# Kernel optimization log

Hardware: AMD Instinct MI355X
Metric: run time of the kernel (lower is better)

Reference implementation:

```python
import jax, jax.numpy as jnp
import numpy as np

D, H, L, V, BS = 1024, 16, 12, 50257, 2048
HD = D // H
EPS = 1e-5


def _ln(x, w, b):
    m = jnp.mean(x, -1, keepdims=True)
    v = jnp.mean(jnp.square(x - m), -1, keepdims=True)
    return (x - m) * jax.lax.rsqrt(v + EPS) * w + b


def setup_inputs() -> dict:
    key = jax.random.key(0)
    ks = jax.random.split(key, 10)
    B, T = 4, 1024
    s = 0.02
    return {
        "idx": jax.random.randint(ks[0], (B, T), 0, V),
        "targets": jax.random.randint(ks[1], (B, T), 0, V),
        "wte": s * jax.random.normal(ks[2], (V, D), jnp.float32),
        "wpe": s * jax.random.normal(ks[3], (BS, D), jnp.float32),
        "ln1_w": jnp.ones((L, D), jnp.float32),
        "ln1_b": jnp.zeros((L, D), jnp.float32),
        "qkv_w": s * jax.random.normal(ks[4], (L, D, 3 * D), jnp.float32),
        "qkv_b": jnp.zeros((L, 3 * D), jnp.float32),
        "o_w": s * jax.random.normal(ks[5], (L, D, D), jnp.float32),
        "o_b": jnp.zeros((L, D), jnp.float32),
        "ln2_w": jnp.ones((L, D), jnp.float32),
        "ln2_b": jnp.zeros((L, D), jnp.float32),
        "up_w": s * jax.random.normal(ks[6], (L, D, 4 * D), jnp.float32),
        "up_b": jnp.zeros((L, 4 * D), jnp.float32),
        "down_w": s * jax.random.normal(ks[7], (L, 4 * D, D), jnp.float32),
        "down_b": jnp.zeros((L, D), jnp.float32),
        "lnf_w": jnp.ones((D,), jnp.float32),
        "lnf_b": jnp.zeros((D,), jnp.float32),
        "lm_b": jnp.zeros((V,), jnp.float32),
    }


def _gpt(idx, targets, wte, wpe, ln1_w, ln1_b, qkv_w, qkv_b, o_w, o_b,
         ln2_w, ln2_b, up_w, up_b, down_w, down_b, lnf_w, lnf_b, lm_b):
    B, T = idx.shape
    x = wte[idx] + wpe[:T][None, :, :]  # [B,T,D]
    causal = jnp.tril(jnp.ones((T, T), bool))
    scale = HD ** -0.5

    def block(h, p):
        (l1w, l1b, qw, qb, ow, ob, l2w, l2b, uw, ub, dw, db) = p
        y = _ln(h, l1w, l1b)
        qkv = y @ qw + qb  # [B,T,3D]
        q, k, v = jnp.split(qkv, 3, axis=-1)
        q = q.reshape(B, T, H, HD)
        k = k.reshape(B, T, H, HD)
        v = v.reshape(B, T, H, HD)
        scores = jnp.einsum('bqhd,bkhd->bhqk', q, k) * scale
        scores = jnp.where(causal, scores, -jnp.inf)
        attn = jax.nn.softmax(scores, axis=-1)
        o = jnp.einsum('bhqk,bkhd->bqhd', attn, v).reshape(B, T, D)
        h = h + o @ ow + ob
        y = _ln(h, l2w, l2b)
        y = jax.nn.gelu(y @ uw + ub, approximate=False)
        h = h + y @ dw + db
        return h, None

    params = (ln1_w, ln1_b, qkv_w, qkv_b, o_w, o_b, ln2_w, ln2_b, up_w, up_b, down_w, down_b)
    x, _ = jax.lax.scan(block, x, params)
    x = _ln(x, lnf_w, lnf_b)
    logits = x @ wte.T + lm_b  # tied lm_head weight
    logp = jax.nn.log_softmax(logits, axis=-1)
    nll = -jnp.take_along_axis(logp, targets[..., None], axis=-1)[..., 0]
    loss = jnp.mean(nll)
    return logits, loss


def reference(idx, targets, wte, wpe, ln1_w, ln1_b, qkv_w, qkv_b, o_w, o_b,
              ln2_w, ln2_b, up_w, up_b, down_w, down_b, lnf_w, lnf_b, lm_b):
    return _gpt(idx, targets, wte, wpe, ln1_w, ln1_b, qkv_w, qkv_b, o_w, o_b,
                ln2_w, ln2_b, up_w, up_b, down_w, down_b, lnf_w, lnf_b, lm_b)
```

## Files before the change

kernel.cpp:

```cpp
#include <hip/hip_runtime.h>
#include <hip/hip_bf16.h>
#include <math.h>

typedef __attribute__((ext_vector_type(8))) short bfrag;
typedef __attribute__((ext_vector_type(4))) float f32x4;

static constexpr int Dm = 1024, Hh = 16, HD = 64, Ll = 12, Tt = 1024, Bb = 4;
static constexpr int Vv = 50257, Mrows = 4096;
static constexpr int PLD = 200;

__device__ inline unsigned short f2bf(float f) {
    unsigned u = __float_as_uint(f);
    u += 0x7fffu + ((u >> 16) & 1u);
    return (unsigned short)(u >> 16);
}
__device__ inline float bf2f(unsigned short s) {
    return __uint_as_float(((unsigned)s) << 16);
}

__device__ inline void gload16(const unsigned short* g, unsigned short* l) {
    __builtin_amdgcn_global_load_lds(
        (const __attribute__((address_space(1))) void*)g,
        (__attribute__((address_space(3))) void*)l, 16, 0, 0);
}

__global__ __launch_bounds__(256)
void embed_kernel(float* __restrict__ x, const float* __restrict__ wte,
                  const float* __restrict__ wpe, const int* __restrict__ idx) {
    int row = blockIdx.x;
    int t = row & (Tt - 1);
    int id = idx[row];
    int c = threadIdx.x * 4;
    float4 a = *reinterpret_cast<const float4*>(&wte[(size_t)id * Dm + c]);
    float4 p = *reinterpret_cast<const float4*>(&wpe[(size_t)t * Dm + c]);
    float4 o;
    o.x = a.x + p.x; o.y = a.y + p.y; o.z = a.z + p.z; o.w = a.w + p.w;
    *reinterpret_cast<float4*>(&x[(size_t)row * Dm + c]) = o;
}

__global__ __launch_bounds__(256)
void ln_kernel(unsigned short* __restrict__ y, const float* __restrict__ x,
               const float* __restrict__ w, const float* __restrict__ b) {
    int row = blockIdx.x;
    int tid = threadIdx.x;
    int lane = tid & 63, wv = tid >> 6;
    const float* xr = x + (size_t)row * Dm;
    float4 v = *reinterpret_cast<const float4*>(&xr[tid * 4]);
    float s1 = v.x + v.y + v.z + v.w;
    float s2 = v.x * v.x + v.y * v.y + v.z * v.z + v.w * v.w;
#pragma unroll
    for (int off = 1; off < 64; off <<= 1) {
        s1 += __shfl_xor(s1, off);
        s2 += __shfl_xor(s2, off);
    }
    __shared__ float r1[4], r2[4];
    if (lane == 0) { r1[wv] = s1; r2[wv] = s2; }
    __syncthreads();
    s1 = r1[0] + r1[1] + r1[2] + r1[3];
    s2 = r2[0] + r2[1] + r2[2] + r2[3];
    float mean = s1 * (1.0f / Dm);
    float var = s2 * (1.0f / Dm) - mean * mean;
    float rstd = rsqrtf(var + 1e-5f);
    float4 wvv = *reinterpret_cast<const float4*>(&w[tid * 4]);
    float4 bv = *reinterpret_cast<const float4*>(&b[tid * 4]);
    ushort4 o;
    o.x = f2bf((v.x - mean) * rstd * wvv.x + bv.x);
    o.y = f2bf((v.y - mean) * rstd * wvv.y + bv.y);
    o.z = f2bf((v.z - mean) * rstd * wvv.z + bv.z);
    o.w = f2bf((v.w - mean) * rstd * wvv.w + bv.w);
    *reinterpret_cast<ushort4*>(&y[(size_t)row * Dm + tid * 4]) = o;
}

__global__ __launch_bounds__(256)
void transpose_layer(const float* __restrict__ qw, const float* __restrict__ ow,
                     const float* __restrict__ uw, const float* __restrict__ dw,
                     unsigned short* __restrict__ wTq, unsigned short* __restrict__ wTo,
                     unsigned short* __restrict__ wTu, unsigned short* __restrict__ wTd) {
    __shared__ float t[32][33];
    int tb = blockIdx.x;
    const float* src; unsigned short* dst; int K, N, nx, base;
    if (tb < 3072)      { src = qw; dst = wTq; K = 1024; N = 3072; nx = 96;  base = 0; }
    else if (tb < 4096) { src = ow; dst = wTo; K = 1024; N = 1024; nx = 32;  base = 3072; }
    else if (tb < 8192) { src = uw; dst = wTu; K = 1024; N = 4096; nx = 128; base = 4096; }
    else                { src = dw; dst = wTd; K = 4096; N = 1024; nx = 32;  base = 8192; }
    int tt = tb - base;
    int n0 = (tt % nx) * 32, k0 = (tt / nx) * 32;
    int tid = threadIdx.x;
    int r = tid >> 3, c4 = (tid & 7) * 4;
    float4 v = *reinterpret_cast<const float4*>(&src[(size_t)(k0 + r) * N + n0 + c4]);
    t[r][c4] = v.x; t[r][c4 + 1] = v.y; t[r][c4 + 2] = v.z; t[r][c4 + 3] = v.w;
    __syncthreads();
    int nr = tid >> 3, kc = (tid & 7) * 4;
    ushort4 o;
    o.x = f2bf(t[kc][nr]);
    o.y = f2bf(t[kc + 1][nr]);
    o.z = f2bf(t[kc + 2][nr]);
    o.w = f2bf(t[kc + 3][nr]);
    *reinterpret_cast<ushort4*>(&dst[(size_t)(n0 + nr) * K + k0 + kc]) = o;
}

__global__ __launch_bounds__(128)
void cvt_rows(unsigned short* __restrict__ dst, const float* __restrict__ src) {
    int row = blockIdx.x;
    int t = threadIdx.x;
    const float* s = src + (size_t)row * Dm + t * 8;
    float4 f0 = *reinterpret_cast<const float4*>(s);
    float4 f1 = *reinterpret_cast<const float4*>(s + 4);
    ushort4 o0, o1;
    o0.x = f2bf(f0.x); o0.y = f2bf(f0.y); o0.z = f2bf(f0.z); o0.w = f2bf(f0.w);
    o1.x = f2bf(f1.x); o1.y = f2bf(f1.y); o1.z = f2bf(f1.z); o1.w = f2bf(f1.w);
    unsigned short* d = dst + (size_t)row * Dm + t * 8;
    *reinterpret_cast<ushort4*>(d) = o0;
    *reinterpret_cast<ushort4*>(d + 4) = o1;
}

template<int EPI, int GN>
__global__ __launch_bounds__(512, 1)
void gemm256p8(const unsigned short* __restrict__ A, const unsigned short* __restrict__ B,
               const float* __restrict__ bias, void* __restrict__ Cp,
               int Nv, int K, int ldc, int ncol,
               float* __restrict__ pm_out, float* __restrict__ ps_out) {
    __shared__ unsigned short AL[2][2][8192];
    __shared__ unsigned short BL[2][2][8192];
    const int tid = threadIdx.x;
    const int lane = tid & 63, w = tid >> 6;
    const int wr = w >> 2, wc = w & 3;
    const int g = lane >> 4, lr = lane & 15;

    const int gx = gridDim.x;
    const int ny = GN ? ((Nv + 255) >> 8) : (int)gridDim.y;
    int s = blockIdx.y * gx + blockIdx.x;
    int xcd = s & 7, t0b = s >> 3;
    int xblk = t0b % gx, istr = t0b / gx;
    int y = xcd + (istr << 3);
    if (GN && y >= ny) return;
    const int bm = xblk * 256;
    const int bn = y * 256;

    const int srow = tid >> 3;
    const int gsrc = (tid & 7) ^ (srow & 7);
    size_t aofs[2][2], bofs[2][2];
#pragma unroll
    for (int h = 0; h < 2; ++h)
#pragma unroll
        for (int j = 0; j < 2; ++j) {
            int ra = bm + h * 128 + srow + j * 64;
            aofs[h][j] = (size_t)ra * K + gsrc * 8;
            int rb = bn + h * 128 + srow + j * 64;
            if (GN) rb = (rb < Nv) ? rb : (Nv - 1);
            bofs[h][j] = (size_t)rb * K + gsrc * 8;
        }
    const int dst0 = tid * 8, dst1 = tid * 8 + 4096;

    const int nt = K >> 6;
    const int ni = nt >> 1;

    f32x4 acc[8][4];
#pragma unroll
    for (int i = 0; i < 8; ++i)
#pragma unroll
        for (int j = 0; j < 4; ++j)
#pragma unroll
            for (int r = 0; r < 4; ++r) acc[i][j][r] = 0.f;

#define STG_A(d, h, kt) do { \
        gload16(A + aofs[h][0] + ((size_t)(kt) << 6), &AL[d][h][dst0]); \
        gload16(A + aofs[h][1] + ((size_t)(kt) << 6), &AL[d][h][dst1]); } while (0)
#define STG_B(d, h, kt) do { \
        gload16(B + bofs[h][0] + ((size_t)(kt) << 6), &BL[d][h][dst0]); \
        gload16(B + bofs[h][1] + ((size_t)(kt) << 6), &BL[d][h][dst1]); } while (0)

    STG_B(0, 0, 0); STG_B(0, 1, 0);
    STG_A(0, 0, 0); STG_A(0, 1, 0);
    STG_B(1, 0, 1); STG_B(1, 1, 1);
    asm volatile("s_waitcnt vmcnt(0)" ::: "memory");
    asm volatile("s_barrier" ::: "memory");

    const unsigned short* alw[2] = { &AL[0][wr][0], &AL[1][wr][0] };
    const unsigned short* blw[2] = { &BL[0][wc >> 1][0], &BL[1][wc >> 1][0] };
    const int rbB = (wc & 1) * 64;

    bfrag bfr[4][2], afr[2][2];

    for (int i = 0; i < ni; ++i) {
        const int t1 = 2 * i + 1;
        const int tp0 = 2 * i + 2, tp1 = 2 * i + 3;
        const bool pf = (tp0 < nt);
#pragma unroll
        for (int q = 0; q < 4; ++q) {
            if (q == 0) {
#pragma unroll
                for (int n_ = 0; n_ < 4; ++n_)
#pragma unroll
                    for (int ks = 0; ks < 2; ++ks) {
                        int row = rbB + n_ * 16 + lr;
                        int sg = (ks * 4 + g) ^ (row & 7);
                        bfr[n_][ks] = *reinterpret_cast<const bfrag*>(&blw[0][row * 64 + sg * 8]);
                    }
            }
#pragma unroll
            for (int m2 = 0; m2 < 2; ++m2)
#pragma unroll
                for (int ks = 0; ks < 2; ++ks) {
                    int row = q * 32 + m2 * 16 + lr;
                    int sg = (ks * 4 + g) ^ (row & 7);
                    afr[m2][ks] = *reinterpret_cast<const bfrag*>(&alw[0][row * 64 + sg * 8]);
                }
            if (q == 0)      { STG_A(1, 0, t1); }
            else if (q == 1) { STG_A(1, 1, t1); }
            else if (q == 2) { if (pf) STG_B(0, 0, tp0); }
            else             { if (pf) STG_B(0, 1, tp0); }
            asm volatile("s_barrier" ::: "memory");
            __builtin_amdgcn_s_setprio(1);
#pragma unroll
            for (int m2 = 0; m2 < 2; ++m2)
#pragma unroll
                for (int n_ = 0; n_ < 4; ++n_)
#pragma unroll
                    for (int ks = 0; ks < 2; ++ks)
                        acc[q * 2 + m2][n_] = __builtin_amdgcn_mfma_f32_16x16x32_bf16(
                            afr[m2][ks], bfr[n_][ks], acc[q * 2 + m2][n_], 0, 0, 0);
            __builtin_amdgcn_s_setprio(0);
            if (q == 3) {
                if (i + 1 < ni) asm volatile("s_waitcnt vmcnt(4)" ::: "memory");
                else            asm volatile("s_waitcnt vmcnt(0)" ::: "memory");
            }
            asm volatile("s_barrier" ::: "memory");
        }
#pragma unroll
        for (int q = 0; q < 4; ++q) {
            if (q == 0) {
#pragma unroll
                for (int n_ = 0; n_ < 4; ++n_)
#pragma unroll
                    for (int ks = 0; ks < 2; ++ks) {
                        int row = rbB + n_ * 16 + lr;
                        int sg = (ks * 4 + g) ^ (row & 7);
                        bfr[n_][ks] = *reinterpret_cast<const bfrag*>(&blw[1][row * 64 + sg * 8]);
                    }
            }
#pragma unroll
            for (int m2 = 0; m2 < 2; ++m2)
#pragma unroll
                for (int ks = 0; ks < 2; ++ks) {
                    int row = q * 32 + m2 * 16 + lr;
                    int sg = (ks * 4 + g) ^ (row & 7);
                    afr[m2][ks] = *reinterpret_cast<const bfrag*>(&alw[1][row * 64 + sg * 8]);
                }
            if (q == 0)      { if (pf) STG_A(0, 0, tp0); }
            else if (q == 1) { if (pf) STG_A(0, 1, tp0); }
            else if (q == 2) { if (tp1 < nt) STG_B(1, 0, tp1); }
            else             { if (tp1 < nt) STG_B(1, 1, tp1); }
            asm volatile("s_barrier" ::: "memory");
            __builtin_amdgcn_s_setprio(1);
#pragma unroll
            for (int m2 = 0; m2 < 2; ++m2)
#pragma unroll
                for (int n_ = 0; n_ < 4; ++n_)
#pragma unroll
                    for (int ks = 0; ks < 2; ++ks)
                        acc[q * 2 + m2][n_] = __builtin_amdgcn_mfma_f32_16x16x32_bf16(
                            afr[m2][ks], bfr[n_][ks], acc[q * 2 + m2][n_], 0, 0, 0);
            __builtin_amdgcn_s_setprio(0);
            if (q == 3 && i + 1 < ni) asm volatile("s_waitcnt vmcnt(4)" ::: "memory");
            asm volatile("s_barrier" ::: "memory");
        }
    }
#undef STG_A
#undef STG_B

    unsigned short* Cb = (unsigned short*)Cp;
    float* Cf = (float*)Cp;

    if (EPI == 1) {
#pragma unroll
        for (int n_ = 0; n_ < 4; ++n_) {
            int col = bn + wc * 64 + n_ * 16 + lr;
            int gcol = ncol + col;
            float bi = bias[gcol];
#pragma unroll
            for (int mi = 0; mi < 8; ++mi) {
                int row0 = bm + wr * 128 + mi * 16 + g * 4;
#pragma unroll
                for (int r = 0; r < 4; ++r) {
                    int row = row0 + r;
                    float v = acc[mi][n_][r] + bi;
                    v = 0.5f * v * (1.0f + erff(v * 0.70710678118654752f));
                    Cb[(size_t)row * ldc + gcol] = f2bf(v);
                }
            }
        }
    } else {
        __syncthreads();
        float* lm = (float*)&AL[0][0][0];
        float* lsd = lm + 1024;
        float bi4[4];
        int colv[4];
#pragma unroll
        for (int n_ = 0; n_ < 4; ++n_) {
            colv[n_] = bn + wc * 64 + n_ * 16 + lr;
            bi4[n_] = (colv[n_] < Nv) ? bias[ncol + colv[n_]] : 0.f;
        }
#pragma unroll
        for (int mi = 0; mi < 8; ++mi) {
#pragma unroll
            for (int r = 0; r < 4; ++r) {
                int row = bm + wr * 128 + mi * 16 + g * 4 + r;
                float vv[4];
                float ml = -3.0e38f, sl = 0.f;
#pragma unroll
                for (int n_ = 0; n_ < 4; ++n_) {
                    float v = acc[mi][n_][r] + bi4[n_];
                    vv[n_] = v;
                    if (colv[n_] < Nv) ml = fmaxf(ml, v);
                }
#pragma unroll
                for (int n_ = 0; n_ < 4; ++n_) {
                    if (colv[n_] < Nv) {
                        sl += __expf(vv[n_] - ml);
                        __builtin_nontemporal_store(
                            vv[n_], &Cf[(size_t)row * ldc + ncol + colv[n_]]);
                    }
                }
#pragma unroll
                for (int off = 1; off < 16; off <<= 1) {
                    float om = __shfl_xor(ml, off);
                    float os = __shfl_xor(sl, off);
                    float nm = fmaxf(ml, om);
                    sl = sl * __expf(ml - nm) + os * __expf(om - nm);
                    ml = nm;
                }
                if (lr == 0) {
                    int lrow = wr * 128 + mi * 16 + g * 4 + r;
                    lm[lrow * 4 + wc] = ml;
                    lsd[lrow * 4 + wc] = sl;
                }
            }
        }
        __syncthreads();
        if (tid < 256) {
            float m0 = lm[tid * 4 + 0], m1 = lm[tid * 4 + 1];
            float m2 = lm[tid * 4 + 2], m3 = lm[tid * 4 + 3];
            float M = fmaxf(fmaxf(m0, m1), fmaxf(m2, m3));
            float S = lsd[tid * 4 + 0] * __expf(m0 - M) + lsd[tid * 4 + 1] * __expf(m1 - M)
                    + lsd[tid * 4 + 2] * __expf(m2 - M) + lsd[tid * 4 + 3] * __expf(m3 - M);
            int row = bm + tid;
            int bno = bn >> 8;
            pm_out[(size_t)row * PLD + bno] = M;
            ps_out[(size_t)row * PLD + bno] = S;
        }
    }
}

template<int EPI>
__global__ __launch_bounds__(256, 2)
void gemm128p(const unsigned short* __restrict__ A, const unsigned short* __restrict__ B,
              const float* __restrict__ bias, const float* __restrict__ R,
              void* __restrict__ Cp, int K, int ldc) {
    __shared__ unsigned short As[4][128 * 32];
    __shared__ unsigned short Bs[4][128 * 32];
    const int tid = threadIdx.x;
    const int lane = tid & 63, w = tid >> 6;
    const int wr = w >> 1, wc = w & 1;
    const int g = lane >> 4, lr = lane & 15;
    const int slotk = (lr >> 1) & 3;

    const int gx = gridDim.x;
    int s = blockIdx.y * gx + blockIdx.x;
    int xcd = s & 7, t0 = s >> 3;
    int xblk = t0 % gx, istr = t0 / gx;
    int y = xcd + (istr << 3);
    const int bm = xblk * 128;
    const int bn = y * 128;

    const int srow = lane >> 2;
    const int gsrc = (lane & 3) ^ ((lane >> 3) & 3);
    const int rA0 = (w * 2 + 0) * 16 + srow;
    const int rA1 = (w * 2 + 1) * 16 + srow;
    const size_t aoff0 = (size_t)(bm + rA0) * K + gsrc * 8;
    const size_t aoff1 = (size_t)(bm + rA1) * K + gsrc * 8;
    const size_t boff0 = (size_t)(bn + rA0) * K + gsrc * 8;
    const size_t boff1 = (size_t)(bn + rA1) * K + gsrc * 8;
    unsigned short* lA0 = &As[0][(w * 2 + 0) * 512];
    unsigned short* lA1 = &As[0][(w * 2 + 1) * 512];
    unsigned short* lB0 = &Bs[0][(w * 2 + 0) * 512];
    unsigned short* lB1 = &Bs[0][(w * 2 + 1) * 512];

    const int nt = K >> 5;

    f32x4 acc[4][4];
#pragma unroll
    for (int i = 0; i < 4; ++i)
#pragma unroll
        for (int j = 0; j < 4; ++j)
#pragma unroll
            for (int r = 0; r < 4; ++r) acc[i][j][r] = 0.f;

#pragma unroll
    for (int tp = 0; tp < 3; ++tp) {
        const int kp = tp << 5;
        gload16(A + aoff0 + kp, lA0 + tp * 4096);
        gload16(B + boff0 + kp, lB0 + tp * 4096);
        gload16(A + aoff1 + kp, lA1 + tp * 4096);
        gload16(B + boff1 + kp, lB1 + tp * 4096);
    }
    asm volatile("s_waitcnt vmcnt(8)" ::: "memory");
    asm volatile("s_barrier" ::: "memory");

    for (int t = 0; t < nt; ++t) {
        const int bt = t & 3;
        const unsigned short* as = As[bt];
        const unsigned short* bs = Bs[bt];
        const int pf = t + 3;
        const int kp = pf << 5;
        const int so = (pf & 3) * 4096;

        bfrag af[4], bfr[4];
#pragma unroll
        for (int i = 0; i < 4; ++i) {
            int ra = wr * 64 + i * 16 + lr;
            af[i] = *reinterpret_cast<const bfrag*>(&as[ra * 32 + ((g ^ slotk) * 8)]);
            int rb = wc * 64 + i * 16 + lr;
            bfr[i] = *reinterpret_cast<const bfrag*>(&bs[rb * 32 + ((g ^ slotk) * 8)]);
        }
        if (pf < nt) {
            gload16(A + aoff0 + kp, lA0 + so);
            gload16(B + boff0 + kp, lB0 + so);
            gload16(A + aoff1 + kp, lA1 + so);
            gload16(B + boff1 + kp, lB1 + so);
        }
        __builtin_amdgcn_s_setprio(1);
#pragma unroll
        for (int mi = 0; mi < 4; ++mi)
#pragma unroll
            for (int ni = 0; ni < 4; ++ni)
                acc[mi][ni] = __builtin_amdgcn_mfma_f32_16x16x32_bf16(
                    af[mi], bfr[ni], acc[mi][ni], 0, 0, 0);
        __builtin_amdgcn_s_setprio(0);
        if (t + 3 < nt)      asm volatile("s_waitcnt vmcnt(8)" ::: "memory");
        else if (t + 2 < nt) asm volatile("s_waitcnt vmcnt(4)" ::: "memory");
        else if (t + 1 < nt) asm volatile("s_waitcnt vmcnt(0)" ::: "memory");
        asm volatile("s_barrier" ::: "memory");
    }

    unsigned short* Cb = (unsigned short*)Cp;
    float* Cf = (float*)Cp;
#pragma unroll
    for (int ni = 0; ni < 4; ++ni) {
        int col = bn + wc * 64 + ni * 16 + lr;
        float bi = bias[col];
#pragma unroll
        for (int mi = 0; mi < 4; ++mi) {
            int row0 = bm + wr * 64 + mi * 16 + g * 4;
#pragma unroll
            for (int r = 0; r < 4; ++r) {
                int row = row0 + r;
                float v = acc[mi][ni][r] + bi;
                if (EPI == 0) {
                    Cb[(size_t)row * ldc + col] = f2bf(v);
                } else {
                    Cf[(size_t)row * ldc + col] = R[(size_t)row * ldc + col] + v;
                }
            }
        }
    }
}

__global__ __launch_bounds__(256)
void attn_mfma(const unsigned short* __restrict__ qkv, unsigned short* __restrict__ ob) {
    const int bq = blockIdx.x;
    const int h = blockIdx.y;
    const int b = blockIdx.z;
    const int tid = threadIdx.x, lane = tid & 63, w = tid >> 6;
    const int g = lane >> 4, lr = lane & 15;
    const int qg0 = bq * 128 + w * 32;

    __shared__ unsigned short Kt[64 * 72];
    __shared__ unsigned short Vt[64 * 72];
    __shared__ unsigned short Pl[4][32 * 72];
    unsigned short* Plw = Pl[w];

    bfrag aq[2][2];
#pragma unroll
    for (int qs = 0; qs < 2; ++qs)
#pragma unroll
        for (int ks = 0; ks < 2; ++ks) {
            int row = qg0 + qs * 16 + lr;
            aq[qs][ks] = *reinterpret_cast<const bfrag*>(
                &qkv[(size_t)(b * Tt + row) * 3072 + h * 64 + ks * 32 + g * 8]);
        }

    float mrow[2][4], lrow[2][4], osc[2][4];
    f32x4 oacc[2][4];
#pragma unroll
    for (int qs = 0; qs < 2; ++qs)
#pragma unroll
        for (int r = 0; r < 4; ++r) { mrow[qs][r] = -3.0e38f; lrow[qs][r] = 0.f; }
#pragma unroll
    for (int qs = 0; qs < 2; ++qs)
#pragma unroll
        for (int dn = 0; dn < 4; ++dn)
#pragma unroll
            for (int r = 0; r < 4; ++r) oacc[qs][dn][r] = 0.f;

    const int ntile = 2 * bq + 2;
    for (int kt = 0; kt < ntile; ++kt) {
        {
            int row = tid >> 2, seg = tid & 3;
            const unsigned short* sk =
                &qkv[(size_t)(b * Tt + kt * 64 + row) * 3072 + Dm + h * 64 + seg * 16];
            bfrag kv0 = *(const bfrag*)sk;
            bfrag kv1 = *(const bfrag*)(sk + 8);
            *reinterpret_cast<bfrag*>(&Kt[row * 72 + seg * 16]) = kv0;
            *reinterpret_cast<bfrag*>(&Kt[row * 72 + seg * 16 + 8]) = kv1;
            const uint4* sv = reinterpret_cast<const uint4*>(
                &qkv[(size_t)(b * Tt + kt * 64 + row) * 3072 + 2 * Dm + h * 64 + seg * 16]);
            uint4 u0 = sv[0], u1 = sv[1];
            uint4 a, r0, r1;
            a.x = (seg & 1) ? u0.y : u0.x; a.y = (seg & 1) ? u0.z : u0.y;
            a.z = (seg & 1) ? u0.w : u0.z; a.w = (seg & 1) ? u0.x : u0.w;
            r0.x = (seg & 2) ? a.z : a.x; r0.y = (seg & 2) ? a.w : a.y;
            r0.z = (seg & 2) ? a.x : a.z; r0.w = (seg & 2) ? a.y : a.w;
            a.x = (seg & 1) ? u1.y : u1.x; a.y = (seg & 1) ? u1.z : u1.y;
            a.z = (seg & 1) ? u1.w : u1.z; a.w = (seg & 1) ? u1.x : u1.w;
            r1.x = (seg & 2) ? a.z : a.x; r1.y = (seg & 2) ? a.w : a.y;
            r1.z = (seg & 2) ? a.x : a.z; r1.w = (seg & 2) ? a.y : a.w;
            unsigned w0[4] = {r0.x, r0.y, r0.z, r0.w};
            unsigned w1[4] = {r1.x, r1.y, r1.z, r1.w};
#pragma unroll
            for (int i = 0; i < 8; ++i) {
                int j = (i + 2 * seg) & 7;
                unsigned ww = w0[i >> 1];
                unsigned short val = (i & 1) ? (unsigned short)(ww >> 16)
                                             : (unsigned short)(ww & 0xffff);
                Vt[(seg * 16 + j) * 72 + row] = val;
            }
#pragma unroll
            for (int i = 0; i < 8; ++i) {
                int j = (i + 2 * seg) & 7;
                unsigned ww = w1[i >> 1];
                unsigned short val = (i & 1) ? (unsigned short)(ww >> 16)
                                             : (unsigned short)(ww & 0xffff);
                Vt[(seg * 16 + 8 + j) * 72 + row] = val;
            }
        }
        __syncthreads();

        bool active = (kt * 64 <= qg0 + 31);
        if (active) {
            f32x4 s[2][4];
#pragma unroll
            for (int qs = 0; qs < 2; ++qs)
#pragma unroll
                for (int n = 0; n < 4; ++n)
#pragma unroll
                    for (int r = 0; r < 4; ++r) s[qs][n][r] = 0.f;
            bfrag bk[4][2];
#pragma unroll
            for (int n = 0; n < 4; ++n)
#pragma unroll
                for (int ks = 0; ks < 2; ++ks)
                    bk[n][ks] = *reinterpret_cast<const bfrag*>(
                        &Kt[(n * 16 + lr) * 72 + ks * 32 + g * 8]);
#pragma unroll
            for (int qs = 0; qs < 2; ++qs)
#pragma unroll
                for (int n = 0; n < 4; ++n)
#pragma unroll
                    for (int ks = 0; ks < 2; ++ks)
                        s[qs][n] = __builtin_amdgcn_mfma_f32_16x16x32_bf16(
                            aq[qs][ks], bk[n][ks], s[qs][n], 0, 0, 0);

            bool mayMask = (kt * 64 + 63 > qg0);
            float pv[2][4][4];
#pragma unroll
            for (int qs = 0; qs < 2; ++qs) {
#pragma unroll
                for (int r = 0; r < 4; ++r) {
                    int qrow = qg0 + qs * 16 + g * 4 + r;
                    float v[4];
#pragma unroll
                    for (int n = 0; n < 4; ++n) {
                        float sv = s[qs][n][r] * 0.125f;
                        if (mayMask && (kt * 64 + n * 16 + lr > qrow)) sv = -3.0e38f;
                        v[n] = sv;
                    }
                    float tmax = fmaxf(fmaxf(v[0], v[1]), fmaxf(v[2], v[3]));
                    tmax = fmaxf(tmax, __shfl_xor(tmax, 1));
                    tmax = fmaxf(tmax, __shfl_xor(tmax, 2));
                    tmax = fmaxf(tmax, __shfl_xor(tmax, 4));
                    tmax = fmaxf(tmax, __shfl_xor(tmax, 8));
                    float mold = mrow[qs][r];
                    float mnew = fmaxf(mold, tmax);
                    float scl = expf(mold - mnew);
                    float psum = 0.f;
#pragma unroll
                    for (int n = 0; n < 4; ++n) {
                        float p = expf(v[n] - mnew);
                        pv[qs][n][r] = p;
                        psum += p;
                    }
                    psum += __shfl_xor(psum, 1);
                    psum += __shfl_xor(psum, 2);
                    psum += __shfl_xor(psum, 4);
                    psum += __shfl_xor(psum, 8);
                    lrow[qs][r] = lrow[qs][r] * scl + psum;
                    mrow[qs][r] = mnew;
                    osc[qs][r] = scl;
                }
            }
#pragma unroll
            for (int qs = 0; qs < 2; ++qs)
#pragma unroll
                for (int dn = 0; dn < 4; ++dn)
#pragma unroll
                    for (int r = 0; r < 4; ++r) oacc[qs][dn][r] *= osc[qs][r];
#pragma unroll
            for (int qs = 0; qs < 2; ++qs)
#pragma unroll
                for (int n = 0; n < 4; ++n)
#pragma unroll
                    for (int r = 0; r < 4; ++r)
                        Plw[(qs * 16 + g * 4 + r) * 72 + n * 16 + lr] = f2bf(pv[qs][n][r]);
            asm volatile("s_waitcnt lgkmcnt(0)" ::: "memory");
            bfrag ap[2][2], bv[4][2];
#pragma unroll
            for (int qs = 0; qs < 2; ++qs)
#pragma unroll
                for (int ks = 0; ks < 2; ++ks)
                    ap[qs][ks] = *reinterpret_cast<const bfrag*>(
                        &Plw[(qs * 16 + lr) * 72 + ks * 32 + g * 8]);
#pragma unroll
            for (int dn = 0; dn < 4; ++dn)
#pragma unroll
                for (int ks = 0; ks < 2; ++ks)
                    bv[dn][ks] = *reinterpret_cast<const bfrag*>(
                        &Vt[(dn * 16 + lr) * 72 + ks * 32 + g * 8]);
#pragma unroll
            for (int qs = 0; qs < 2; ++qs)
#pragma unroll
                for (int dn = 0; dn < 4; ++dn)
#pragma unroll
                    for (int ks = 0; ks < 2; ++ks)
                        oacc[qs][dn] = __builtin_amdgcn_mfma_f32_16x16x32_bf16(
                            ap[qs][ks], bv[dn][ks], oacc[qs][dn], 0, 0, 0);
        }
        __syncthreads();
    }

#pragma unroll
    for (int qs = 0; qs < 2; ++qs)
#pragma unroll
        for (int r = 0; r < 4; ++r) {
            float rinv = 1.0f / lrow[qs][r];
            int qrow = qg0 + qs * 16 + g * 4 + r;
#pragma unroll
            for (int dn = 0; dn < 4; ++dn)
                ob[(size_t)(b * Tt + qrow) * Dm + h * 64 + dn * 16 + lr] =
                    f2bf(oacc[qs][dn][r] * rinv);
        }
}

__global__ __launch_bounds__(64)
void loss_combine(float* __restrict__ nll, const float* __restrict__ pm,
                  const float* __restrict__ ps, const float* __restrict__ logits,
                  const int* __restrict__ targets, int nby) {
    const int row = blockIdx.x;
    const int lane = threadIdx.x;
    float m = -3.0e38f, s = 0.f;
    for (int j = lane; j < nby; j += 64) {
        float om = pm[(size_t)row * PLD + j];
        float os = ps[(size_t)row * PLD + j];
        float nm = fmaxf(m, om);
        s = s * __expf(m - nm) + os * __expf(om - nm);
        m = nm;
    }
#pragma unroll
    for (int off = 1; off < 64; off <<= 1) {
        float om = __shfl_xor(m, off);
        float os = __shfl_xor(s, off);
        float nm = fmaxf(m, om);
        s = s * __expf(m - nm) + os * __expf(om - nm);
        m = nm;
    }
    if (lane == 0) {
        float lse = m + __logf(s);
        nll[row] = lse - logits[(size_t)row * Vv + targets[row]];
    }
}

__global__ __launch_bounds__(256)
void loss_reduce_kernel(float* __restrict__ loss, const float* __restrict__ nll) {
    int tid = threadIdx.x;
    __shared__ float red[256];
    float s = 0.f;
    for (int j = tid; j < Mrows; j += 256) s += nll[j];
    red[tid] = s;
    __syncthreads();
    for (int st = 128; st > 0; st >>= 1) {
        if (tid < st) red[tid] += red[tid + st];
        __syncthreads();
    }
    if (tid == 0) *loss = red[0] * (1.0f / Mrows);
}

extern "C" void kernel_launch(void* const* d_in, const int* in_sizes, int n_in,
                              void* d_out, int out_size, void* d_ws, size_t ws_size,
                              hipStream_t stream) {
    const int* idx = (const int*)d_in[0];
    const int* targets = (const int*)d_in[1];
    const float* wte = (const float*)d_in[2];
    const float* wpe = (const float*)d_in[3];
    const float* ln1_w = (const float*)d_in[4];
    const float* ln1_b = (const float*)d_in[5];
    const float* qkv_w = (const float*)d_in[6];
    const float* qkv_b = (const float*)d_in[7];
    const float* o_w = (const float*)d_in[8];
    const float* o_b = (const float*)d_in[9];
    const float* ln2_w = (const float*)d_in[10];
    const float* ln2_b = (const float*)d_in[11];
    const float* up_w = (const float*)d_in[12];
    const float* up_b = (const float*)d_in[13];
    const float* down_w = (const float*)d_in[14];
    const float* down_b = (const float*)d_in[15];
    const float* lnf_w = (const float*)d_in[16];
    const float* lnf_b = (const float*)d_in[17];
    const float* lm_b = (const float*)d_in[18];

    float* logits = (float*)d_out;
    char* ws = (char*)d_ws;
    const size_t MB = 1 << 20;
    float* x            = (float*)(ws);
    unsigned short* y   = (unsigned short*)(ws + 16 * MB);
    unsigned short* qkv = (unsigned short*)(ws + 24 * MB);
    unsigned short* ob  = (unsigned short*)(ws + 48 * MB);
    unsigned short* up  = (unsigned short*)(ws + 56 * MB);
    unsigned short* wTq = (unsigned short*)(ws + 88 * MB);
    unsigned short* wTo = (unsigned short*)(ws + 96 * MB);
    unsigned short* wTu = (unsigned short*)(ws + 100 * MB);
    unsigned short* wTd = (unsigned short*)(ws + 112 * MB);
    float* nll          = (float*)(ws + 127 * MB);
    unsigned short* wbf = (unsigned short*)(ws + 24 * MB);
    float* pmp          = (float*)(ws + 131 * MB);
    float* psp          = (float*)(ws + 136 * MB);

    embed_kernel<<<Mrows, 256, 0, stream>>>(x, wte, wpe, idx);

    for (int l = 0; l < Ll; ++l) {
        ln_kernel<<<Mrows, 256, 0, stream>>>(y, x, ln1_w + l * Dm, ln1_b + l * Dm);
        transpose_layer<<<12288, 256, 0, stream>>>(
            qkv_w + (size_t)l * Dm * 3 * Dm, o_w + (size_t)l * Dm * Dm,
            up_w + (size_t)l * Dm * 4 * Dm, down_w + (size_t)l * 4 * Dm * Dm,
            wTq, wTo, wTu, wTd);
        gemm128p<0><<<dim3(Mrows / 128, 3 * Dm / 128), 256, 0, stream>>>(
            y, wTq, qkv_b + (size_t)l * 3 * Dm, nullptr, qkv, Dm, 3 * Dm);
        attn_mfma<<<dim3(8, Hh, Bb), 256, 0, stream>>>(qkv, ob);
        gemm128p<2><<<dim3(Mrows / 128, Dm / 128), 256, 0, stream>>>(
            ob, wTo, o_b + (size_t)l * Dm, x, x, Dm, Dm);
        ln_kernel<<<Mrows, 256, 0, stream>>>(y, x, ln2_w + l * Dm, ln2_b + l * Dm);
        gemm256p8<1, 0><<<dim3(Mrows / 256, 4 * Dm / 256), 512, 0, stream>>>(
            y, wTu, up_b + (size_t)l * 4 * Dm, up, 4 * Dm, Dm, 4 * Dm, 0,
            nullptr, nullptr);
        gemm128p<2><<<dim3(Mrows / 128, Dm / 128), 256, 0, stream>>>(
            up, wTd, down_b + (size_t)l * Dm, x, x, 4 * Dm, Dm);
    }

    ln_kernel<<<Mrows, 256, 0, stream>>>(y, x, lnf_w, lnf_b);

    cvt_rows<<<Vv, 128, 0, stream>>>(wbf, wte);
    const int NBY = (Vv + 255) / 256;
    const int NBY_PAD = ((NBY + 7) / 8) * 8;
    gemm256p8<4, 1><<<dim3(Mrows / 256, NBY_PAD), 512, 0, stream>>>(
        y, wbf, lm_b, logits, Vv, Dm, Vv, 0, pmp, psp);

    loss_combine<<<Mrows, 64, 0, stream>>>(nll, pmp, psp, logits, targets, NBY);
    loss_reduce_kernel<<<1, 256, 0, stream>>>(logits + (size_t)Mrows * Vv, nll);
}
```

Baseline: 4.300 ms.

## Stage LM-head logits through LDS for coalesced stores; nontemporal A loads

In the LM-head GEMM epilogue, logits are written into an LDS staging buffer in 64-row chunks, then stored to global memory as contiguous rows, replacing the scattered per-fragment nontemporal stores. The shared A/B buffers are merged into one array so the staging area and the max/sum scratch can reuse it. For the vocab GEMM, A-operand loads also use a nontemporal cache hint. This targets poorly coalesced writes of the large fp32 logits tensor, at the cost of extra barriers and LDS traffic in the epilogue.

```diff
diff --git a/kernel.cpp b/kernel.cpp
--- a/kernel.cpp
+++ b/kernel.cpp
@@ -22,6 +22,11 @@
     __builtin_amdgcn_global_load_lds(
         (const __attribute__((address_space(1))) void*)g,
         (__attribute__((address_space(3))) void*)l, 16, 0, 0);
+}
+__device__ inline void gload16nt(const unsigned short* g, unsigned short* l) {
+    __builtin_amdgcn_global_load_lds(
+        (const __attribute__((address_space(1))) void*)g,
+        (__attribute__((address_space(3))) void*)l, 16, 0, 2 );
 }
 
 __global__ __launch_bounds__(256)
@@ -120,8 +125,9 @@
                const float* __restrict__ bias, void* __restrict__ Cp,
                int Nv, int K, int ldc, int ncol,
                float* __restrict__ pm_out, float* __restrict__ ps_out) {
-    __shared__ unsigned short AL[2][2][8192];
-    __shared__ unsigned short BL[2][2][8192];
+    __shared__ unsigned short SH[2][2][2][8192];
+#define AL_(d, h) (&SH[0][d][h][0])
+#define BL_(d, h) (&SH[1][d][h][0])
     const int tid = threadIdx.x;
     const int lane = tid & 63, w = tid >> 6;
     const int wr = w >> 2, wc = w & 3;
@@ -164,11 +170,15 @@
             for (int r = 0; r < 4; ++r) acc[i][j][r] = 0.f;
 
 #define STG_A(d, h, kt) do { \
-        gload16(A + aofs[h][0] + ((size_t)(kt) << 6), &AL[d][h][dst0]); \
-        gload16(A + aofs[h][1] + ((size_t)(kt) << 6), &AL[d][h][dst1]); } while (0)
+        if (GN) { \
+            gload16nt(A + aofs[h][0] + ((size_t)(kt) << 6), AL_(d, h) + dst0); \
+            gload16nt(A + aofs[h][1] + ((size_t)(kt) << 6), AL_(d, h) + dst1); \
+        } else { \
+            gload16(A + aofs[h][0] + ((size_t)(kt) << 6), AL_(d, h) + dst0); \
+            gload16(A + aofs[h][1] + ((size_t)(kt) << 6), AL_(d, h) + dst1); } } while (0)
 #define STG_B(d, h, kt) do { \
-        gload16(B + bofs[h][0] + ((size_t)(kt) << 6), &BL[d][h][dst0]); \
-        gload16(B + bofs[h][1] + ((size_t)(kt) << 6), &BL[d][h][dst1]); } while (0)
+        gload16(B + bofs[h][0] + ((size_t)(kt) << 6), BL_(d, h) + dst0); \
+        gload16(B + bofs[h][1] + ((size_t)(kt) << 6), BL_(d, h) + dst1); } while (0)
 
     STG_B(0, 0, 0); STG_B(0, 1, 0);
     STG_A(0, 0, 0); STG_A(0, 1, 0);
@@ -176,8 +186,8 @@
     asm volatile("s_waitcnt vmcnt(0)" ::: "memory");
     asm volatile("s_barrier" ::: "memory");
 
-    const unsigned short* alw[2] = { &AL[0][wr][0], &AL[1][wr][0] };
-    const unsigned short* blw[2] = { &BL[0][wc >> 1][0], &BL[1][wc >> 1][0] };
+    const unsigned short* alw[2] = { AL_(0, wr), AL_(1, wr) };
+    const unsigned short* blw[2] = { BL_(0, wc >> 1), BL_(1, wc >> 1) };
     const int rbB = (wc & 1) * 64;
 
     bfrag bfr[4][2], afr[2][2];
@@ -292,7 +302,8 @@
         }
     } else {
         __syncthreads();
-        float* lm = (float*)&AL[0][0][0];
+        float* scs = (float*)&SH[0][0][0][0];
+        float* lm = scs + 64 * 258;
         float* lsd = lm + 1024;
         float bi4[4];
         int colv[4];
@@ -301,43 +312,61 @@
             colv[n_] = bn + wc * 64 + n_ * 16 + lr;
             bi4[n_] = (colv[n_] < Nv) ? bias[ncol + colv[n_]] : 0.f;
         }
-#pragma unroll
-        for (int mi = 0; mi < 8; ++mi) {
-#pragma unroll
-            for (int r = 0; r < 4; ++r) {
-                int row = bm + wr * 128 + mi * 16 + g * 4 + r;
-                float vv[4];
-                float ml = -3.0e38f, sl = 0.f;
-#pragma unroll
-                for (int n_ = 0; n_ < 4; ++n_) {
-                    float v = acc[mi][n_][r] + bi4[n_];
-                    vv[n_] = v;
-                    if (colv[n_] < Nv) ml = fmaxf(ml, v);
-                }
-#pragma unroll
-                for (int n_ = 0; n_ < 4; ++n_) {
-                    if (colv[n_] < Nv) {
-                        sl += __expf(vv[n_] - ml);
-                        __builtin_nontemporal_store(
-                            vv[n_], &Cf[(size_t)row * ldc + ncol + colv[n_]]);
+        const int cbase = ncol + bn;
+        const bool full = (bn + 256 <= Nv);
+        for (int c = 0; c < 4; ++c) {
+            if (wr == (c >> 1)) {
+                const int mib = (c & 1) * 4;
+#pragma unroll
+                for (int mr = 0; mr < 4; ++mr) {
+                    const int mi = mib + mr;
+#pragma unroll
+                    for (int r = 0; r < 4; ++r) {
+                        int row_l = mr * 16 + g * 4 + r;
+                        float vv[4];
+                        float ml = -3.0e38f, sl = 0.f;
+#pragma unroll
+                        for (int n_ = 0; n_ < 4; ++n_) {
+                            float v = acc[mi][n_][r] + bi4[n_];
+                            vv[n_] = v;
+                            if (colv[n_] < Nv) ml = fmaxf(ml, v);
+                        }
+#pragma unroll
+                        for (int n_ = 0; n_ < 4; ++n_) {
+                            if (colv[n_] < Nv) sl += __expf(vv[n_] - ml);
+                            scs[row_l * 258 + wc * 64 + n_ * 16 + lr] = vv[n_];
+                        }
+#pragma unroll
+                        for (int off = 1; off < 16; off <<= 1) {
+                            float om = __shfl_xor(ml, off);
+                            float os = __shfl_xor(sl, off);
+                            float nm = fmaxf(ml, om);
+                            sl = sl * __expf(ml - nm) + os * __expf(om - nm);
+                            ml = nm;
+                        }
+                        if (lr == 0) {
+                            int lrow = (c >> 1) * 128 + mi * 16 + g * 4 + r;
+                            lm[lrow * 4 + wc] = ml;
+                            lsd[lrow * 4 + wc] = sl;
+                        }
                     }
                 }
-#pragma unroll
-                for (int off = 1; off < 16; off <<= 1) {
-                    float om = __shfl_xor(ml, off);
-                    float os = __shfl_xor(sl, off);
-                    float nm = fmaxf(ml, om);
-                    sl = sl * __expf(ml - nm) + os * __expf(om - nm);
-                    ml = nm;
+            }
+            __syncthreads();
+            const int rowg0 = bm + c * 64;
+#pragma unroll
+            for (int j = 0; j < 32; ++j) {
+                int idx = tid + j * 512;
+                int rl = idx >> 8;
+                int cl = idx & 255;
+                if (full || (bn + cl) < Nv) {
+                    float v = scs[rl * 258 + cl];
+                    __builtin_nontemporal_store(
+                        v, &Cf[(size_t)(rowg0 + rl) * ldc + cbase + cl]);
                 }
-                if (lr == 0) {
-                    int lrow = wr * 128 + mi * 16 + g * 4 + r;
-                    lm[lrow * 4 + wc] = ml;
-                    lsd[lrow * 4 + wc] = sl;
-                }
-            }
-        }
-        __syncthreads();
+            }
+            __syncthreads();
+        }
         if (tid < 256) {
             float m0 = lm[tid * 4 + 0], m1 = lm[tid * 4 + 1];
             float m2 = lm[tid * 4 + 2], m3 = lm[tid * 4 + 3];
@@ -350,6 +379,8 @@
             ps_out[(size_t)row * PLD + bno] = S;
         }
     }
+#undef AL_
+#undef BL_
 }
 
 template<int EPI>
```

Result: slower. 4.618 ms (+7.4%).
